# Performance work log

Hardware: AMD Instinct MI355X
Metric: run time of the kernel (lower is better)

Reference implementation:

```python
import jax, jax.numpy as jnp
import numpy as np

EMBED_DIM = 2048
NUM_HEADS = 16
HEAD_DIM = EMBED_DIM // NUM_HEADS  # 128
D_K = 128
SCALE = 1.0 / float(np.sqrt(HEAD_DIM))
LAYER_DEPTH = 6 / 12  # amrpa_layer_idx / n_amrpa_layers
BATCH, SEQ = 2, 2048


def setup_inputs() -> dict:
    key = jax.random.key(0)
    ks = jax.random.split(key, 8)
    return {
        "hidden_states": jax.random.normal(ks[0], (BATCH, SEQ, EMBED_DIM), jnp.float32),
        "c_attn_w": jax.random.normal(ks[1], (EMBED_DIM, 3 * EMBED_DIM), jnp.float32) * 0.02,
        "c_attn_b": jax.random.normal(ks[2], (3 * EMBED_DIM,), jnp.float32) * 0.02,
        "c_proj_w": jax.random.normal(ks[3], (EMBED_DIM, EMBED_DIM), jnp.float32) * 0.02,
        "c_proj_b": jax.random.normal(ks[4], (EMBED_DIM,), jnp.float32) * 0.02,
        "cam_gate": jax.random.normal(ks[5], (D_K,), jnp.float32) * 0.1,
        "cam_w0": jax.random.normal(ks[6], (1,), jnp.float32),
        "cam_w1": jax.random.normal(ks[7], (1,), jnp.float32),
    }


def reference(hidden_states, c_attn_w, c_attn_b, c_proj_w, c_proj_b, cam_gate, cam_w0, cam_w1):
    # GPT2 Conv1D-style fused QKV projection: [B,S,3E]
    qkv = hidden_states @ c_attn_w + c_attn_b
    Q, K, V = jnp.split(qkv, 3, axis=2)  # each [B,S,E]
    # NOTE: faithful to source — attention over the FULL embed dim (no head split),
    # scaled by 1/sqrt(head_dim); causal mask is computed but never applied upstream.
    attn_scores = jnp.einsum('bse,bte->bst', Q, K) * SCALE  # [B,S,S]

    # CAM: sliced low-rank channels
    Q_cam, K_cam, V_cam = Q[:, :, :D_K], K[:, :, :D_K], V[:, :, :D_K]
    # base attention map computed under no_grad in the original
    base_A = jax.lax.stop_gradient(
        jax.nn.softmax(jnp.einsum('bsd,btd->bst', Q_cam, K_cam) * SCALE, axis=-1))
    layer_weight = jax.nn.sigmoid(cam_w0[0] + cam_w1[0] * LAYER_DEPTH)
    cam_ctx = jnp.einsum('bst,btd->bsd', base_A, V_cam)            # [B,S,d_k]
    cam_bias = jnp.einsum('bsd,btd->bst', jnp.tanh(cam_ctx * cam_gate), K_cam)
    cam_bias = cam_bias * (SCALE * layer_weight)                   # cam_mask is all-ones

    final_attn = jax.nn.softmax(attn_scores + cam_bias, axis=-1)
    context = jnp.einsum('bst,bte->bse', final_attn, V)            # [B,S,E]
    output = context @ c_proj_w + c_proj_b                         # resid_dropout is identity (eval)
    return output
```

## Files before the change

### kernel.cpp

```cpp
#include <hip/hip_runtime.h>
#include <hip/hip_bf16.h>

typedef unsigned short u16;
typedef __attribute__((ext_vector_type(8))) __bf16 bf16x8;
typedef __attribute__((ext_vector_type(4))) float f32x4;
typedef __attribute__((ext_vector_type(4))) unsigned short u16x4;

#define SCALE_QK 0.08838834764831845f

__device__ __forceinline__ u16 f2bf(float x) {
  union { float f; unsigned u; } v; v.f = x;
  unsigned r = v.u + 0x7fffu + ((v.u >> 16) & 1u);
  return (u16)(r >> 16);
}

__device__ __forceinline__ void gload_lds16(const u16* g, u16* l) {
  __builtin_amdgcn_global_load_lds(
      (const __attribute__((address_space(1))) unsigned*)g,
      (__attribute__((address_space(3))) unsigned*)l, 16, 0, 0);
}

#define CFENCE() asm volatile("" ::: "memory")
#define WAITV(N) asm volatile("s_waitcnt vmcnt(" #N ")" ::: "memory")

template<bool OUT_BF16, bool HAS_BIAS, bool TWO_SEG>
__global__ __launch_bounds__(512, 2)
void g128p(const u16* __restrict__ A1, int lda1, long sA1,
           const u16* __restrict__ B1, int ldb1, long sB1, int K1,
           const u16* __restrict__ A2, int lda2, long sA2,
           const u16* __restrict__ B2, int ldb2, long sB2, int K2,
           void* __restrict__ Cv, int ldc, long sC,
           float scale, const float* __restrict__ bias, int nbx)
{
  extern __shared__ u16 lds[];
  const int bz = blockIdx.z;
  const int nwg = gridDim.x, orig = blockIdx.x;
  const int q8 = nwg >> 3, r8 = nwg & 7;
  const int xcd = orig & 7, lp = orig >> 3;
  const int wg = (xcd < r8 ? xcd * (q8 + 1) : r8 * (q8 + 1) + (xcd - r8) * q8) + lp;
  const int bx = wg % nbx, by = wg / nbx;
  const long m0 = (long)by * 256, n0 = (long)bx * 128;

  const int tid = threadIdx.x, wid = tid >> 6, lane = tid & 63;
  const int wm = wid >> 1, wn = wid & 1;
  const int rl = lane & 15, g = lane >> 4;
  const int sw = ((g ^ ((rl >> 1) & 3)) << 3);

  int aoff[4], boff[4];
#pragma unroll
  for (int i = 0; i < 4; ++i) aoff[i] = (wm * 64 + i * 16 + rl) * 32 + sw;
#pragma unroll
  for (int j = 0; j < 4; ++j) boff[j] = (wn * 64 + j * 16 + rl) * 32 + sw;

  const int srow = tid >> 2;
  const int scolX = (((tid & 3) ^ ((srow >> 1) & 3)) << 3);

  f32x4 acc[4][4];
#pragma unroll
  for (int i = 0; i < 4; ++i)
#pragma unroll
    for (int j = 0; j < 4; ++j) acc[i][j] = (f32x4){0.f, 0.f, 0.f, 0.f};

  bf16x8 avA[4], bvA[4], avB[4], bvB[4];

#define STG(H_) {                                                        \
    const int h_ = (H_);                                                 \
    const u16* sa_ = Ab + (long)srow * lda + h_ * 32 + scolX;            \
    u16* da_ = lds + ((h_ & 3) * 8192) + tid * 8;                        \
    gload_lds16(sa_, da_);                                               \
    gload_lds16(sa_ + (long)128 * lda, da_ + 4096);                      \
    gload_lds16(Bb + (long)srow * ldb + h_ * 32 + scolX,                 \
                lds + 32768 + ((h_ & 3) * 4096) + tid * 8); }
#define RD(H_, AV, BV) {                                                 \
    const u16* aS_ = lds + (((H_) & 3) * 8192);                          \
    const u16* bS_ = lds + 32768 + (((H_) & 3) * 4096);                  \
    _Pragma("unroll") for (int i_ = 0; i_ < 4; ++i_)                     \
      AV[i_] = *(const bf16x8*)(aS_ + aoff[i_]);                         \
    _Pragma("unroll") for (int j_ = 0; j_ < 4; ++j_)                     \
      BV[j_] = *(const bf16x8*)(bS_ + boff[j_]); }
#define BODY(K_, CAV, CBV, NAV, NBV, W_STMT, DO_RD, DO_ST)               \
    W_STMT;                                                              \
    CFENCE(); __builtin_amdgcn_s_barrier(); CFENCE();                    \
    asm volatile("s_waitcnt lgkmcnt(0)" ::: "memory");                   \
    __builtin_amdgcn_sched_barrier(0);                                   \
    __builtin_amdgcn_s_setprio(1);                                       \
    _Pragma("unroll") for (int i_ = 0; i_ < 4; ++i_)                     \
      _Pragma("unroll") for (int j_ = 0; j_ < 4; ++j_)                   \
        acc[i_][j_] = __builtin_amdgcn_mfma_f32_16x16x32_bf16(           \
            CAV[i_], CBV[j_], acc[i_][j_], 0, 0, 0);                     \
    __builtin_amdgcn_s_setprio(0);                                       \
    if (DO_RD) { RD((K_) + 1, NAV, NBV); }                               \
    if (DO_ST) { STG((K_) + 4); }                                        \
    CFENCE();

  const int NSEG = TWO_SEG ? 2 : 1;
#pragma unroll 1
  for (int seg = 0; seg < NSEG; ++seg) {
    const int lda = (seg == 0) ? lda1 : lda2;
    const int ldb = (seg == 0) ? ldb1 : ldb2;
    const int K   = (seg == 0) ? K1 : K2;
    const u16* Ab = ((seg == 0) ? A1 + (long)bz * sA1 : A2 + (long)bz * sA2) + m0 * (long)lda;
    const u16* Bb = ((seg == 0) ? B1 + (long)bz * sB1 : B2 + (long)bz * sB2) + n0 * (long)ldb;
    const int H = K >> 5;

    STG(0); STG(1); STG(2);
    WAITV(6);
    CFENCE(); __builtin_amdgcn_s_barrier(); CFENCE();
    RD(0, avA, bvA);
    STG(3);
    CFENCE();

#pragma unroll 1
    for (int k = 0; k + 5 < H; k += 2) {
      BODY(k,     avA, bvA, avB, bvB, WAITV(6), true, true);
      BODY(k + 1, avB, bvB, avA, bvA, WAITV(6), true, true);
    }
    BODY(H - 4, avA, bvA, avB, bvB, WAITV(6), true,  false);
    BODY(H - 3, avB, bvB, avA, bvA, WAITV(3), true,  false);
    BODY(H - 2, avA, bvA, avB, bvB, WAITV(0), true,  false);
    BODY(H - 1, avB, bvB, avA, bvA, (void)0,  false, false);
  }
#undef STG
#undef RD
#undef BODY

  const int r0 = (lane >> 4) << 2;
  const int cL = lane & 15;
#pragma unroll
  for (int i = 0; i < 4; ++i) {
#pragma unroll
    for (int j = 0; j < 4; ++j) {
      const long row = m0 + wm * 64 + i * 16 + r0;
      const long col = n0 + wn * 64 + j * 16 + cL;
      float bvs = 0.f;
      if (HAS_BIAS) bvs = bias[col];
      if (OUT_BF16) {
        u16* Cp = (u16*)Cv + (long)bz * sC;
#pragma unroll
        for (int r = 0; r < 4; ++r)
          Cp[(row + r) * ldc + col] = f2bf(acc[i][j][r] * scale + bvs);
      } else {
        float* Cp = (float*)Cv + (long)bz * sC;
#pragma unroll
        for (int r = 0; r < 4; ++r)
          Cp[(row + r) * ldc + col] = acc[i][j][r] * scale + bvs;
      }
    }
  }
}

template<bool OUT_BF16, bool HAS_BIAS>
__global__ __launch_bounds__(256)
void gemm_bt(const u16* __restrict__ A, int lda, long sA,
             const u16* __restrict__ B, int ldb, long sB,
             void* __restrict__ Cv, int ldc, long sC,
             int K, float scale, const float* __restrict__ bias)
{
  __shared__ u16 As[128 * 64];
  __shared__ u16 Bs[128 * 64];
  const int bz   = blockIdx.z;
  const u16* Ap  = A + (long)bz * sA;
  const u16* Bp  = B + (long)bz * sB;
  const int tid  = threadIdx.x;
  const int wid  = tid >> 6;
  const int lane = tid & 63;
  const long m0  = (long)blockIdx.y * 128;
  const long n0  = (long)blockIdx.x * 128;
  const int lrow = lane >> 3;
  const int lk   = (lane & 7) << 3;
  const int wr   = wid >> 1, wc = wid & 1;

  f32x4 acc[4][4];
#pragma unroll
  for (int i = 0; i < 4; ++i)
#pragma unroll
    for (int j = 0; j < 4; ++j) acc[i][j] = (f32x4){0.f, 0.f, 0.f, 0.f};

  for (int k0 = 0; k0 < K; k0 += 64) {
#pragma unroll
    for (int c4 = 0; c4 < 4; ++c4) {
      const int chunk = (wid << 2) + c4;
      gload_lds16(Ap + (m0 + (chunk << 3) + lrow) * lda + k0 + lk, &As[chunk << 9]);
      gload_lds16(Bp + (n0 + (chunk << 3) + lrow) * ldb + k0 + lk, &Bs[chunk << 9]);
    }
    __syncthreads();
#pragma unroll
    for (int kk = 0; kk < 2; ++kk) {
      bf16x8 af[4], bfr[4];
      const int kof   = (kk << 5) + ((lane >> 4) << 3);
      const int rbase = lane & 15;
#pragma unroll
      for (int i = 0; i < 4; ++i)
        af[i] = *(const bf16x8*)&As[(((wr << 6) + (i << 4) + rbase) << 6) + kof];
#pragma unroll
      for (int j = 0; j < 4; ++j)
        bfr[j] = *(const bf16x8*)&Bs[(((wc << 6) + (j << 4) + rbase) << 6) + kof];
#pragma unroll
      for (int i = 0; i < 4; ++i)
#pragma unroll
        for (int j = 0; j < 4; ++j)
          acc[i][j] = __builtin_amdgcn_mfma_f32_16x16x32_bf16(af[i], bfr[j], acc[i][j], 0, 0, 0);
    }
    __syncthreads();
  }

  const int r0 = (lane >> 4) << 2;
  const int cL = lane & 15;
#pragma unroll
  for (int i = 0; i < 4; ++i) {
#pragma unroll
    for (int j = 0; j < 4; ++j) {
      const long row = m0 + (wr << 6) + (i << 4) + r0;
      const long col = n0 + (wc << 6) + (j << 4) + cL;
      float bv = 0.f;
      if (HAS_BIAS) bv = bias[col];
      if (OUT_BF16) {
        u16* Cp = (u16*)Cv + (long)bz * sC;
#pragma unroll
        for (int r = 0; r < 4; ++r)
          Cp[(row + r) * ldc + col] = f2bf(acc[i][j][r] * scale + bv);
      } else {
        float* Cp = (float*)Cv + (long)bz * sC;
#pragma unroll
        for (int r = 0; r < 4; ++r)
          Cp[(row + r) * ldc + col] = acc[i][j][r] * scale + bv;
      }
    }
  }
}

__global__ __launch_bounds__(256)
void gemm_bt_splitk(const u16* __restrict__ A, int lda, long sA,
                    const u16* __restrict__ B, int ldb, long sB,
                    float* __restrict__ C, int ldc, long sC,
                    int Kslice, float scale)
{
  __shared__ u16 As[128 * 64];
  __shared__ u16 Bs[128 * 64];
  const int ks = blockIdx.z & 7;
  const int bz = blockIdx.z >> 3;
  const u16* Ap  = A + (long)bz * sA + ks * Kslice;
  const u16* Bp  = B + (long)bz * sB + ks * Kslice;
  const int tid  = threadIdx.x;
  const int wid  = tid >> 6;
  const int lane = tid & 63;
  const long m0  = (long)blockIdx.y * 128;
  const long n0  = (long)blockIdx.x * 128;
  const int lrow = lane >> 3;
  const int lk   = (lane & 7) << 3;
  const int wr   = wid >> 1, wc = wid & 1;

  f32x4 acc[4][4];
#pragma unroll
  for (int i = 0; i < 4; ++i)
#pragma unroll
    for (int j = 0; j < 4; ++j) acc[i][j] = (f32x4){0.f, 0.f, 0.f, 0.f};

  for (int k0 = 0; k0 < Kslice; k0 += 64) {
#pragma unroll
    for (int c4 = 0; c4 < 4; ++c4) {
      const int chunk = (wid << 2) + c4;
      gload_lds16(Ap + (m0 + (chunk << 3) + lrow) * lda + k0 + lk, &As[chunk << 9]);
      gload_lds16(Bp + (n0 + (chunk << 3) + lrow) * ldb + k0 + lk, &Bs[chunk << 9]);
    }
    __syncthreads();
#pragma unroll
    for (int kk = 0; kk < 2; ++kk) {
      bf16x8 af[4], bfr[4];
      const int kof   = (kk << 5) + ((lane >> 4) << 3);
      const int rbase = lane & 15;
#pragma unroll
      for (int i = 0; i < 4; ++i)
        af[i] = *(const bf16x8*)&As[(((wr << 6) + (i << 4) + rbase) << 6) + kof];
#pragma unroll
      for (int j = 0; j < 4; ++j)
        bfr[j] = *(const bf16x8*)&Bs[(((wc << 6) + (j << 4) + rbase) << 6) + kof];
#pragma unroll
      for (int i = 0; i < 4; ++i)
#pragma unroll
        for (int j = 0; j < 4; ++j)
          acc[i][j] = __builtin_amdgcn_mfma_f32_16x16x32_bf16(af[i], bfr[j], acc[i][j], 0, 0, 0);
    }
    __syncthreads();
  }

  const int r0 = (lane >> 4) << 2;
  const int cL = lane & 15;
  float* Cp = C + (long)bz * sC;
#pragma unroll
  for (int i = 0; i < 4; ++i) {
#pragma unroll
    for (int j = 0; j < 4; ++j) {
      const long row = m0 + (wr << 6) + (i << 4) + r0;
      const long col = n0 + (wc << 6) + (j << 4) + cL;
#pragma unroll
      for (int r = 0; r < 4; ++r)
        atomicAdd(&Cp[(row + r) * ldc + col], acc[i][j][r] * scale);
    }
  }
}

__global__ __launch_bounds__(256)
void softmax_rows2048(const float* __restrict__ src, u16* __restrict__ dst) {
  const long row = blockIdx.x;
  const float4* s = (const float4*)(src + row * 2048);
  const int tid = threadIdx.x;
  float4 a = s[tid * 2], b = s[tid * 2 + 1];
  float m = fmaxf(fmaxf(fmaxf(a.x, a.y), fmaxf(a.z, a.w)),
                  fmaxf(fmaxf(b.x, b.y), fmaxf(b.z, b.w)));
#pragma unroll
  for (int o = 32; o > 0; o >>= 1) m = fmaxf(m, __shfl_xor(m, o));
  __shared__ float redm[4];
  __shared__ float reds[4];
  if ((tid & 63) == 0) redm[tid >> 6] = m;
  __syncthreads();
  m = fmaxf(fmaxf(redm[0], redm[1]), fmaxf(redm[2], redm[3]));
  float e[8];
  e[0] = __expf(a.x - m); e[1] = __expf(a.y - m); e[2] = __expf(a.z - m); e[3] = __expf(a.w - m);
  e[4] = __expf(b.x - m); e[5] = __expf(b.y - m); e[6] = __expf(b.z - m); e[7] = __expf(b.w - m);
  float sum = e[0] + e[1] + e[2] + e[3] + e[4] + e[5] + e[6] + e[7];
#pragma unroll
  for (int o = 32; o > 0; o >>= 1) sum += __shfl_xor(sum, o);
  if ((tid & 63) == 0) reds[tid >> 6] = sum;
  __syncthreads();
  sum = reds[0] + reds[1] + reds[2] + reds[3];
  const float inv = 1.f / sum;
  u16x4 o1 = { f2bf(e[0] * inv), f2bf(e[1] * inv), f2bf(e[2] * inv), f2bf(e[3] * inv) };
  u16x4 o2 = { f2bf(e[4] * inv), f2bf(e[5] * inv), f2bf(e[6] * inv), f2bf(e[7] * inv) };
  u16x4* d = (u16x4*)(dst + row * 2048);
  d[tid * 2]     = o1;
  d[tid * 2 + 1] = o2;
}

__global__ void transpose_f32_to_bf16(const float* __restrict__ src, u16* __restrict__ dst,
                                      int R, int C) {
  __shared__ float t[32][33];
  const int c0 = blockIdx.x * 32, r0 = blockIdx.y * 32;
  const int tx = threadIdx.x, ty = threadIdx.y;
#pragma unroll
  for (int i = 0; i < 4; ++i)
    t[ty + i * 8][tx] = src[(long)(r0 + ty + i * 8) * C + c0 + tx];
  __syncthreads();
#pragma unroll
  for (int i = 0; i < 4; ++i)
    dst[(long)(c0 + ty + i * 8) * R + r0 + tx] = f2bf(t[tx][ty + i * 8]);
}

__global__ void transpose_bf16_batched(const u16* __restrict__ src, int ss, long sbat,
                                       u16* __restrict__ dst, int ds, long dbat) {
  __shared__ u16 t[32][33];
  const u16* s = src + (long)blockIdx.z * sbat;
  u16* d = dst + (long)blockIdx.z * dbat;
  const int c0 = blockIdx.x * 32, r0 = blockIdx.y * 32;
  const int tx = threadIdx.x, ty = threadIdx.y;
#pragma unroll
  for (int i = 0; i < 4; ++i)
    t[ty + i * 8][tx] = s[(long)(r0 + ty + i * 8) * ss + c0 + tx];
  __syncthreads();
#pragma unroll
  for (int i = 0; i < 4; ++i)
    d[(long)(c0 + ty + i * 8) * ds + r0 + tx] = t[tx][ty + i * 8];
}

__global__ __launch_bounds__(256)
void convert_f32_to_bf16(const float* __restrict__ src, u16* __restrict__ dst, long n4) {
  long i = (long)blockIdx.x * 256 + threadIdx.x;
  if (i < n4) {
    float4 v = ((const float4*)src)[i];
    *(u16x4*)(dst + i * 4) = (u16x4){ f2bf(v.x), f2bf(v.y), f2bf(v.z), f2bf(v.w) };
  }
}

__global__ __launch_bounds__(256)
void cam_tanh_kernel(const float* __restrict__ ctx, const float* __restrict__ gate,
                     const float* __restrict__ lw, u16* __restrict__ out, int n) {
  int i = blockIdx.x * 256 + threadIdx.x;
  if (i < n) {
    int d = i & 127;
    out[i] = f2bf(tanhf(ctx[i] * gate[d]) * lw[0]);
  }
}

__global__ __launch_bounds__(256)
void zero_f32(float* __restrict__ p, int n) {
  int i = blockIdx.x * 256 + threadIdx.x;
  if (i < n) p[i] = 0.f;
}

__global__ void calc_lw_kernel(const float* w0, const float* w1, float* lw) {
  *lw = 1.f / (1.f + __expf(-(w0[0] + 0.5f * w1[0])));
}

extern "C" void kernel_launch(void* const* d_in, const int* in_sizes, int n_in,
                              void* d_out, int out_size, void* d_ws, size_t ws_size,
                              hipStream_t stream) {
  const float* hs       = (const float*)d_in[0];
  const float* c_attn_w = (const float*)d_in[1];
  const float* c_attn_b = (const float*)d_in[2];
  const float* c_proj_w = (const float*)d_in[3];
  const float* c_proj_b = (const float*)d_in[4];
  const float* cam_gate = (const float*)d_in[5];
  const float* cam_w0   = (const float*)d_in[6];
  const float* cam_w1   = (const float*)d_in[7];
  float* out = (float*)d_out;

  char* w = (char*)d_ws;
  float* lw      = (float*)(w + 0);
  u16*   hs_b    = (u16*)(w + 256);
  u16*   waT_b   = (u16*)(w + 256 + 16777216UL);
  u16*   wpT_b   = (u16*)(w + 256 + 41943040UL);
  u16*   qkv_b   = (u16*)(w + 256 + 50331648UL);
  u16*   vT_b    = (u16*)(w + 256 + 100663296UL);
  float* scoresF = (float*)(w + 256 + 117440512UL);
  float* camS    = (float*)(w + 256 + 150994944UL);
  float* ctxF    = (float*)(w + 256 + 184549376UL);
  u16*   camT_b  = (u16*)(w + 256 + 186646528UL);
  u16* baseA_b = hs_b;
  u16* P_b     = (u16*)camS;
  u16* ctxE_b  = (u16*)scoresF;

  dim3 b256(256);

  hipFuncSetAttribute((const void*)g128p<true, true, false>,
                      hipFuncAttributeMaxDynamicSharedMemorySize, 98304);
  hipFuncSetAttribute((const void*)g128p<false, false, true>,
                      hipFuncAttributeMaxDynamicSharedMemorySize, 98304);
  hipFuncSetAttribute((const void*)g128p<true, false, false>,
                      hipFuncAttributeMaxDynamicSharedMemorySize, 98304);
  hipFuncSetAttribute((const void*)g128p<false, true, false>,
                      hipFuncAttributeMaxDynamicSharedMemorySize, 98304);

  calc_lw_kernel<<<dim3(1), dim3(1), 0, stream>>>(cam_w0, cam_w1, lw);
  convert_f32_to_bf16<<<dim3(8192), b256, 0, stream>>>(hs, hs_b, 2097152L);
  transpose_f32_to_bf16<<<dim3(192, 64), dim3(32, 8), 0, stream>>>(c_attn_w, waT_b, 2048, 6144);
  transpose_f32_to_bf16<<<dim3(64, 64), dim3(32, 8), 0, stream>>>(c_proj_w, wpT_b, 2048, 2048);

  g128p<true, true, false><<<dim3(768, 1, 1), dim3(512), 98304, stream>>>(
      hs_b, 2048, 0L, waT_b, 2048, 0L, 2048,
      nullptr, 0, 0L, nullptr, 0, 0L, 0,
      qkv_b, 6144, 0L, 1.f, c_attn_b, 48);

  transpose_bf16_batched<<<dim3(64, 64, 2), dim3(32, 8), 0, stream>>>(
      qkv_b + 4096, 6144, 2048L * 6144, vT_b, 2048, 2048L * 2048);

  gemm_bt<false, false><<<dim3(16, 16, 2), b256, 0, stream>>>(
      qkv_b, 6144, 2048L * 6144, qkv_b + 2048, 6144, 2048L * 6144,
      camS, 2048, 2048L * 2048, 128, SCALE_QK, nullptr);

  softmax_rows2048<<<dim3(4096), b256, 0, stream>>>(camS, baseA_b);

  zero_f32<<<dim3(2048), b256, 0, stream>>>(ctxF, 524288);
  gemm_bt_splitk<<<dim3(1, 16, 16), b256, 0, stream>>>(
      baseA_b, 2048, 2048L * 2048, vT_b, 2048, 2048L * 2048,
      ctxF, 128, 2048L * 128, 256, 1.f);

  cam_tanh_kernel<<<dim3(2048), b256, 0, stream>>>(ctxF, cam_gate, lw, camT_b, 524288);

  g128p<false, false, true><<<dim3(128, 1, 2), dim3(512), 98304, stream>>>(
      qkv_b, 6144, 2048L * 6144, qkv_b + 2048, 6144, 2048L * 6144, 2048,
      camT_b, 128, 2048L * 128, qkv_b + 2048, 6144, 2048L * 6144, 128,
      scoresF, 2048, 2048L * 2048, SCALE_QK, nullptr, 16);

  softmax_rows2048<<<dim3(4096), b256, 0, stream>>>(scoresF, P_b);

  g128p<true, false, false><<<dim3(128, 1, 2), dim3(512), 98304, stream>>>(
      P_b, 2048, 2048L * 2048, vT_b, 2048, 2048L * 2048, 2048,
      nullptr, 0, 0L, nullptr, 0, 0L, 0,
      ctxE_b, 2048, 2048L * 2048, 1.f, nullptr, 16);

  g128p<false, true, false><<<dim3(256, 1, 1), dim3(512), 98304, stream>>>(
      ctxE_b, 2048, 0L, wpT_b, 2048, 0L, 2048,
      nullptr, 0, 0L, nullptr, 0, 0L, 0,
      out, 2048, 0L, 1.f, c_proj_b, 16);
}
```

Measured before the change: 348.0 us.

## Switch GEMM to three-stage LDS ring and reuse it for CAM scores

```diff
diff --git a/kernel.cpp b/kernel.cpp
--- a/kernel.cpp
+++ b/kernel.cpp
@@ -25,7 +25,7 @@
 
 template<bool OUT_BF16, bool HAS_BIAS, bool TWO_SEG>
 __global__ __launch_bounds__(512, 2)
-void g128p(const u16* __restrict__ A1, int lda1, long sA1,
+void g128m(const u16* __restrict__ A1, int lda1, long sA1,
            const u16* __restrict__ B1, int ldb1, long sB1, int K1,
            const u16* __restrict__ A2, int lda2, long sA2,
            const u16* __restrict__ B2, int ldb2, long sB2, int K2,
@@ -50,7 +50,7 @@
 #pragma unroll
   for (int i = 0; i < 4; ++i) aoff[i] = (wm * 64 + i * 16 + rl) * 32 + sw;
 #pragma unroll
-  for (int j = 0; j < 4; ++j) boff[j] = (wn * 64 + j * 16 + rl) * 32 + sw;
+  for (int j = 0; j < 4; ++j) boff[j] = 8192 + (wn * 64 + j * 16 + rl) * 32 + sw;
 
   const int srow = tid >> 2;
   const int scolX = (((tid & 3) ^ ((srow >> 1) & 3)) << 3);
@@ -61,37 +61,32 @@
 #pragma unroll
     for (int j = 0; j < 4; ++j) acc[i][j] = (f32x4){0.f, 0.f, 0.f, 0.f};
 
-  bf16x8 avA[4], bvA[4], avB[4], bvB[4];
-
-#define STG(H_) {                                                        \
-    const int h_ = (H_);                                                 \
-    const u16* sa_ = Ab + (long)srow * lda + h_ * 32 + scolX;            \
-    u16* da_ = lds + ((h_ & 3) * 8192) + tid * 8;                        \
+  bf16x8 av[4], bv[4];
+
+#define STG(H_, BS_) {                                                   \
+    const u16* sa_ = Ab + (long)srow * lda + (H_) * 32 + scolX;          \
+    u16* da_ = lds + (BS_) * 12288 + tid * 8;                            \
     gload_lds16(sa_, da_);                                               \
     gload_lds16(sa_ + (long)128 * lda, da_ + 4096);                      \
-    gload_lds16(Bb + (long)srow * ldb + h_ * 32 + scolX,                 \
-                lds + 32768 + ((h_ & 3) * 4096) + tid * 8); }
-#define RD(H_, AV, BV) {                                                 \
-    const u16* aS_ = lds + (((H_) & 3) * 8192);                          \
-    const u16* bS_ = lds + 32768 + (((H_) & 3) * 4096);                  \
+    gload_lds16(Bb + (long)srow * ldb + (H_) * 32 + scolX,               \
+                lds + (BS_) * 12288 + 8192 + tid * 8); }
+#define RD(BT_) {                                                        \
+    const u16* bp_ = lds + (BT_) * 12288;                                \
     _Pragma("unroll") for (int i_ = 0; i_ < 4; ++i_)                     \
-      AV[i_] = *(const bf16x8*)(aS_ + aoff[i_]);                         \
+      av[i_] = *(const bf16x8*)(bp_ + aoff[i_]);                         \
     _Pragma("unroll") for (int j_ = 0; j_ < 4; ++j_)                     \
-      BV[j_] = *(const bf16x8*)(bS_ + boff[j_]); }
-#define BODY(K_, CAV, CBV, NAV, NBV, W_STMT, DO_RD, DO_ST)               \
-    W_STMT;                                                              \
-    CFENCE(); __builtin_amdgcn_s_barrier(); CFENCE();                    \
+      bv[j_] = *(const bf16x8*)(bp_ + boff[j_]); }
+#define MMTAIL()                                                         \
+    CFENCE(); __builtin_amdgcn_s_barrier();                              \
     asm volatile("s_waitcnt lgkmcnt(0)" ::: "memory");                   \
     __builtin_amdgcn_sched_barrier(0);                                   \
     __builtin_amdgcn_s_setprio(1);                                       \
     _Pragma("unroll") for (int i_ = 0; i_ < 4; ++i_)                     \
       _Pragma("unroll") for (int j_ = 0; j_ < 4; ++j_)                   \
         acc[i_][j_] = __builtin_amdgcn_mfma_f32_16x16x32_bf16(           \
-            CAV[i_], CBV[j_], acc[i_][j_], 0, 0, 0);                     \
+            av[i_], bv[j_], acc[i_][j_], 0, 0, 0);                       \
     __builtin_amdgcn_s_setprio(0);                                       \
-    if (DO_RD) { RD((K_) + 1, NAV, NBV); }                               \
-    if (DO_ST) { STG((K_) + 4); }                                        \
-    CFENCE();
+    CFENCE(); __builtin_amdgcn_s_barrier(); CFENCE();
 
   const int NSEG = TWO_SEG ? 2 : 1;
 #pragma unroll 1
@@ -101,28 +96,32 @@
     const int K   = (seg == 0) ? K1 : K2;
     const u16* Ab = ((seg == 0) ? A1 + (long)bz * sA1 : A2 + (long)bz * sA2) + m0 * (long)lda;
     const u16* Bb = ((seg == 0) ? B1 + (long)bz * sB1 : B2 + (long)bz * sB2) + n0 * (long)ldb;
-    const int H = K >> 5;
-
-    STG(0); STG(1); STG(2);
-    WAITV(6);
+    const int NT = K >> 5;
+
+    STG(0, 0); STG(1, 1);
+    WAITV(3);
     CFENCE(); __builtin_amdgcn_s_barrier(); CFENCE();
-    RD(0, avA, bvA);
-    STG(3);
-    CFENCE();
-
+
+    int bt = 0;
 #pragma unroll 1
-    for (int k = 0; k + 5 < H; k += 2) {
-      BODY(k,     avA, bvA, avB, bvB, WAITV(6), true, true);
-      BODY(k + 1, avB, bvB, avA, bvA, WAITV(6), true, true);
-    }
-    BODY(H - 4, avA, bvA, avB, bvB, WAITV(6), true,  false);
-    BODY(H - 3, avB, bvB, avA, bvA, WAITV(3), true,  false);
-    BODY(H - 2, avA, bvA, avB, bvB, WAITV(0), true,  false);
-    BODY(H - 1, avB, bvB, avA, bvA, (void)0,  false, false);
+    for (int t = 0; t < NT - 2; ++t) {
+      const int bs = (bt + 2 >= 3) ? bt - 1 : bt + 2;
+      RD(bt);
+      STG(t + 2, bs);
+      WAITV(3);
+      MMTAIL();
+      bt = (bt + 1 == 3) ? 0 : bt + 1;
+    }
+    RD(bt);
+    WAITV(0);
+    MMTAIL();
+    bt = (bt + 1 == 3) ? 0 : bt + 1;
+    RD(bt);
+    MMTAIL();
   }
 #undef STG
 #undef RD
-#undef BODY
+#undef MMTAIL
 
   const int r0 = (lane >> 4) << 2;
   const int cL = lane & 15;
@@ -144,86 +143,6 @@
 #pragma unroll
         for (int r = 0; r < 4; ++r)
           Cp[(row + r) * ldc + col] = acc[i][j][r] * scale + bvs;
-      }
-    }
-  }
-}
-
-template<bool OUT_BF16, bool HAS_BIAS>
-__global__ __launch_bounds__(256)
-void gemm_bt(const u16* __restrict__ A, int lda, long sA,
-             const u16* __restrict__ B, int ldb, long sB,
-             void* __restrict__ Cv, int ldc, long sC,
-             int K, float scale, const float* __restrict__ bias)
-{
-  __shared__ u16 As[128 * 64];
-  __shared__ u16 Bs[128 * 64];
-  const int bz   = blockIdx.z;
-  const u16* Ap  = A + (long)bz * sA;
-  const u16* Bp  = B + (long)bz * sB;
-  const int tid  = threadIdx.x;
-  const int wid  = tid >> 6;
-  const int lane = tid & 63;
-  const long m0  = (long)blockIdx.y * 128;
-  const long n0  = (long)blockIdx.x * 128;
-  const int lrow = lane >> 3;
-  const int lk   = (lane & 7) << 3;
-  const int wr   = wid >> 1, wc = wid & 1;
-
-  f32x4 acc[4][4];
-#pragma unroll
-  for (int i = 0; i < 4; ++i)
-#pragma unroll
-    for (int j = 0; j < 4; ++j) acc[i][j] = (f32x4){0.f, 0.f, 0.f, 0.f};
-
-  for (int k0 = 0; k0 < K; k0 += 64) {
-#pragma unroll
-    for (int c4 = 0; c4 < 4; ++c4) {
-      const int chunk = (wid << 2) + c4;
-      gload_lds16(Ap + (m0 + (chunk << 3) + lrow) * lda + k0 + lk, &As[chunk << 9]);
-      gload_lds16(Bp + (n0 + (chunk << 3) + lrow) * ldb + k0 + lk, &Bs[chunk << 9]);
-    }
-    __syncthreads();
-#pragma unroll
-    for (int kk = 0; kk < 2; ++kk) {
-      bf16x8 af[4], bfr[4];
-      const int kof   = (kk << 5) + ((lane >> 4) << 3);
-      const int rbase = lane & 15;
-#pragma unroll
-      for (int i = 0; i < 4; ++i)
-        af[i] = *(const bf16x8*)&As[(((wr << 6) + (i << 4) + rbase) << 6) + kof];
-#pragma unroll
-      for (int j = 0; j < 4; ++j)
-        bfr[j] = *(const bf16x8*)&Bs[(((wc << 6) + (j << 4) + rbase) << 6) + kof];
-#pragma unroll
-      for (int i = 0; i < 4; ++i)
-#pragma unroll
-        for (int j = 0; j < 4; ++j)
-          acc[i][j] = __builtin_amdgcn_mfma_f32_16x16x32_bf16(af[i], bfr[j], acc[i][j], 0, 0, 0);
-    }
-    __syncthreads();
-  }
-
-  const int r0 = (lane >> 4) << 2;
-  const int cL = lane & 15;
-#pragma unroll
-  for (int i = 0; i < 4; ++i) {
-#pragma unroll
-    for (int j = 0; j < 4; ++j) {
-      const long row = m0 + (wr << 6) + (i << 4) + r0;
-      const long col = n0 + (wc << 6) + (j << 4) + cL;
-      float bv = 0.f;
-      if (HAS_BIAS) bv = bias[col];
-      if (OUT_BF16) {
-        u16* Cp = (u16*)Cv + (long)bz * sC;
-#pragma unroll
-        for (int r = 0; r < 4; ++r)
-          Cp[(row + r) * ldc + col] = f2bf(acc[i][j][r] * scale + bv);
-      } else {
-        float* Cp = (float*)Cv + (long)bz * sC;
-#pragma unroll
-        for (int r = 0; r < 4; ++r)
-          Cp[(row + r) * ldc + col] = acc[i][j][r] * scale + bv;
       }
     }
   }
@@ -420,22 +339,25 @@
   u16* ctxE_b  = (u16*)scoresF;
 
   dim3 b256(256);
-
-  hipFuncSetAttribute((const void*)g128p<true, true, false>,
-                      hipFuncAttributeMaxDynamicSharedMemorySize, 98304);
-  hipFuncSetAttribute((const void*)g128p<false, false, true>,
-                      hipFuncAttributeMaxDynamicSharedMemorySize, 98304);
-  hipFuncSetAttribute((const void*)g128p<true, false, false>,
-                      hipFuncAttributeMaxDynamicSharedMemorySize, 98304);
-  hipFuncSetAttribute((const void*)g128p<false, true, false>,
-                      hipFuncAttributeMaxDynamicSharedMemorySize, 98304);
+  const int LDSB = 73728;
+
+  hipFuncSetAttribute((const void*)g128m<true, true, false>,
+                      hipFuncAttributeMaxDynamicSharedMemorySize, LDSB);
+  hipFuncSetAttribute((const void*)g128m<false, false, false>,
+                      hipFuncAttributeMaxDynamicSharedMemorySize, LDSB);
+  hipFuncSetAttribute((const void*)g128m<false, false, true>,
+                      hipFuncAttributeMaxDynamicSharedMemorySize, LDSB);
+  hipFuncSetAttribute((const void*)g128m<true, false, false>,
+                      hipFuncAttributeMaxDynamicSharedMemorySize, LDSB);
+  hipFuncSetAttribute((const void*)g128m<false, true, false>,
+                      hipFuncAttributeMaxDynamicSharedMemorySize, LDSB);
 
   calc_lw_kernel<<<dim3(1), dim3(1), 0, stream>>>(cam_w0, cam_w1, lw);
   convert_f32_to_bf16<<<dim3(8192), b256, 0, stream>>>(hs, hs_b, 2097152L);
   transpose_f32_to_bf16<<<dim3(192, 64), dim3(32, 8), 0, stream>>>(c_attn_w, waT_b, 2048, 6144);
   transpose_f32_to_bf16<<<dim3(64, 64), dim3(32, 8), 0, stream>>>(c_proj_w, wpT_b, 2048, 2048);
 
-  g128p<true, true, false><<<dim3(768, 1, 1), dim3(512), 98304, stream>>>(
+  g128m<true, true, false><<<dim3(768, 1, 1), dim3(512), LDSB, stream>>>(
       hs_b, 2048, 0L, waT_b, 2048, 0L, 2048,
       nullptr, 0, 0L, nullptr, 0, 0L, 0,
       qkv_b, 6144, 0L, 1.f, c_attn_b, 48);
@@ -443,9 +365,10 @@
   transpose_bf16_batched<<<dim3(64, 64, 2), dim3(32, 8), 0, stream>>>(
       qkv_b + 4096, 6144, 2048L * 6144, vT_b, 2048, 2048L * 2048);
 
-  gemm_bt<false, false><<<dim3(16, 16, 2), b256, 0, stream>>>(
-      qkv_b, 6144, 2048L * 6144, qkv_b + 2048, 6144, 2048L * 6144,
-      camS, 2048, 2048L * 2048, 128, SCALE_QK, nullptr);
+  g128m<false, false, false><<<dim3(128, 1, 2), dim3(512), LDSB, stream>>>(
+      qkv_b, 6144, 2048L * 6144, qkv_b + 2048, 6144, 2048L * 6144, 128,
+      nullptr, 0, 0L, nullptr, 0, 0L, 0,
+      camS, 2048, 2048L * 2048, SCALE_QK, nullptr, 16);
 
   softmax_rows2048<<<dim3(4096), b256, 0, stream>>>(camS, baseA_b);
 
@@ -456,19 +379,19 @@
 
   cam_tanh_kernel<<<dim3(2048), b256, 0, stream>>>(ctxF, cam_gate, lw, camT_b, 524288);
 
-  g128p<false, false, true><<<dim3(128, 1, 2), dim3(512), 98304, stream>>>(
+  g128m<false, false, true><<<dim3(128, 1, 2), dim3(512), LDSB, stream>>>(
       qkv_b, 6144, 2048L * 6144, qkv_b + 2048, 6144, 2048L * 6144, 2048,
       camT_b, 128, 2048L * 128, qkv_b + 2048, 6144, 2048L * 6144, 128,
       scoresF, 2048, 2048L * 2048, SCALE_QK, nullptr, 16);
 
   softmax_rows2048<<<dim3(4096), b256, 0, stream>>>(scoresF, P_b);
 
-  g128p<true, false, false><<<dim3(128, 1, 2), dim3(512), 98304, stream>>>(
+  g128m<true, false, false><<<dim3(128, 1, 2), dim3(512), LDSB, stream>>>(
       P_b, 2048, 2048L * 2048, vT_b, 2048, 2048L * 2048, 2048,
       nullptr, 0, 0L, nullptr, 0, 0L, 0,
       ctxE_b, 2048, 2048L * 2048, 1.f, nullptr, 16);
 
-  g128p<false, true, false><<<dim3(256, 1, 1), dim3(512), 98304, stream>>>(
+  g128m<false, true, false><<<dim3(256, 1, 1), dim3(512), LDSB, stream>>>(
       ctxE_b, 2048, 0L, wpT_b, 2048, 0L, 2048,
       nullptr, 0, 0L, nullptr, 0, 0L, 0,
       out, 2048, 0L, 1.f, c_proj_b, 16);
```

Result: slower. 360.5 us (+3.6%).
